# Optimization experiments

Hardware: AMD Instinct MI355X
Metric: run time of the kernel (lower is better)

## Reference

```python
import jax, jax.numpy as jnp
import numpy as np

N = 256          # number of samples (each = 3 LSTM steps)
E = 2048         # embedding dim (LSTM input size)
H = 2048         # LSTM hidden dim
CTX_VOCAB = 32
FACE_VOCAB = 1024
OUT_DIM = 2
CTX_SCALE = 1.0


def setup_inputs() -> dict:
    key = jax.random.key(0)
    ks = jax.random.split(key, 12)
    s = 0.02
    inp = {
        "ctx": jax.random.randint(ks[0], (N,), 0, CTX_VOCAB),
        "f1": jax.random.randint(ks[1], (N,), 0, FACE_VOCAB),
        "f2": jax.random.randint(ks[2], (N,), 0, FACE_VOCAB),
        "ctx_table": jax.random.normal(ks[3], (CTX_VOCAB, E), jnp.float32) * s,
        "face_table": jax.random.normal(ks[4], (FACE_VOCAB, E), jnp.float32) * s,
        "W_ih": jax.random.normal(ks[5], (4 * H, E), jnp.float32) * s,
        "W_hh": jax.random.normal(ks[6], (4 * H, H), jnp.float32) * s,
        "b_ih": jax.random.normal(ks[7], (4 * H,), jnp.float32) * s,
        "b_hh": jax.random.normal(ks[8], (4 * H,), jnp.float32) * s,
        "W_out": jax.random.normal(ks[9], (OUT_DIM, H), jnp.float32) * s,
        "b_out": jax.random.normal(ks[10], (OUT_DIM,), jnp.float32) * s,
    }
    return inp


def _lstm_scan(xs, h0, c0, W_ih, W_hh, b_ih, b_hh):
    # xs: [T, E]; single-layer LSTM, batch = 1 (vectors). PyTorch gate order i,f,g,o.
    def step(carry, x):
        h, c = carry
        gates = W_ih @ x + b_ih + W_hh @ h + b_hh  # [4H]
        i, f, g, o = jnp.split(gates, 4)
        i = jax.nn.sigmoid(i)
        f = jax.nn.sigmoid(f)
        g = jnp.tanh(g)
        o = jax.nn.sigmoid(o)
        c = f * c + i * g
        h = o * jnp.tanh(c)
        return (h, c), h

    (hF, cF), hs = jax.lax.scan(step, (h0, c0), xs)
    return hs, hF, cF  # hs: [T, H]


def reference(ctx, f1, f2, ctx_table, face_table, W_ih, W_hh, b_ih, b_hh, W_out, b_out):
    # Per-sample embeddings (batch dim of 1 in original collapses to vectors).
    ctx_e = CTX_SCALE * ctx_table[ctx]          # [N, E]
    f1_e = face_table[f1]                       # [N, E]
    f2_e = face_table[f2]                       # [N, E]
    # ctx_order == 'first': sequence per sample is [ctx, f1, f2].
    x = jnp.stack([ctx_e, f1_e, f2_e], axis=1).reshape(-1, ctx_table.shape[1])  # [3N, E]

    h0 = jnp.zeros((W_hh.shape[1],), x.dtype)
    c0 = jnp.zeros((W_hh.shape[1],), x.dtype)
    hs, hF, cF = _lstm_scan(x, h0, c0, W_ih, W_hh, b_ih, b_hh)

    # Original applies `out` to h_n after each sample (i.e., after its 3rd step).
    h_per_sample = hs[2::3]                     # [N, H]
    outputs = h_per_sample @ W_out.T + b_out    # [N, OUT_DIM]
    return outputs, hF, cF
```

## Files before the change

### kernel.cpp

```cpp
#include <hip/hip_runtime.h>
#include <hip/hip_bf16.h>
#include <stdint.h>

#define H 2048
#define FOURH 8192
#define NT 768
#define NS 256

typedef __attribute__((ext_vector_type(8))) short bf16x8;
typedef __attribute__((ext_vector_type(4))) float f32x4;
typedef __attribute__((ext_vector_type(4))) unsigned uint4v;
typedef _Float16 f16x2 __attribute__((ext_vector_type(2)));

static __device__ __forceinline__ unsigned short f2bf(float x) {
  unsigned u = __float_as_uint(x);
  return (unsigned short)((u + 0x7fffu + ((u >> 16) & 1u)) >> 16);
}
static __device__ __forceinline__ unsigned pk2(float lo, float hi) {
  return ((unsigned)f2bf(hi) << 16) | (unsigned)f2bf(lo);
}
static __device__ __forceinline__ unsigned pkf16(float lo, float hi) {
  auto h = __builtin_amdgcn_cvt_pkrtz(lo, hi);
  return __builtin_bit_cast(unsigned, h);
}
static __device__ __forceinline__ float sigm(float x) { return 1.f / (1.f + __expf(-x)); }
static __device__ __forceinline__ float tanh_fast(float x) {
  float xc = fminf(fmaxf(x, -15.f), 15.f);
  float e = __expf(2.f * xc);
  return (e - 1.f) / (e + 1.f);
}

static __device__ __forceinline__ float dot2(unsigned w, unsigned h, float acc) {
#if __has_builtin(__builtin_amdgcn_fdot2)
  return __builtin_amdgcn_fdot2(__builtin_bit_cast(f16x2, w),
                                __builtin_bit_cast(f16x2, h), acc, false);
#else
  f16x2 wv = __builtin_bit_cast(f16x2, w);
  f16x2 hv = __builtin_bit_cast(f16x2, h);
  return acc + (float)wv.x * (float)hv.x + (float)wv.y * (float)hv.y;
#endif
}

template <int PAT>
static __device__ __forceinline__ float swz(float v) {
  return __int_as_float(__builtin_amdgcn_ds_swizzle(__float_as_int(v), PAT));
}
static __device__ __forceinline__ float wave_sum(float v) {
  v += swz<0x041F>(v);
  v += swz<0x081F>(v);
  v += swz<0x101F>(v);
  v += swz<0x201F>(v);
  v += swz<0x401F>(v);
  v += __shfl_xor(v, 32, 64);
  return v;
}

__global__ void gather_x(const int* __restrict__ ctx, const int* __restrict__ f1,
                         const int* __restrict__ f2, const float* __restrict__ ctx_table,
                         const float* __restrict__ face_table, unsigned short* __restrict__ X) {
  int t = blockIdx.x;
  int s = t / 3, k = t - 3 * s;
  const float* src;
  if (k == 0)      src = ctx_table  + (size_t)ctx[s] * H;
  else if (k == 1) src = face_table + (size_t)f1[s] * H;
  else             src = face_table + (size_t)f2[s] * H;
  int c = threadIdx.x * 8;
  float4 v0 = *(const float4*)(src + c);
  float4 v1 = *(const float4*)(src + c + 4);
  uint4 o;
  o.x = pk2(v0.x, v0.y); o.y = pk2(v0.z, v0.w);
  o.z = pk2(v1.x, v1.y); o.w = pk2(v1.z, v1.w);
  *(uint4*)(X + (size_t)t * H + c) = o;
}

__launch_bounds__(256)
__global__ void gemm_p(const unsigned short* __restrict__ X, const float* __restrict__ Wih,
                       const float* __restrict__ bih, const float* __restrict__ bhh,
                       float* __restrict__ P) {
  __shared__ unsigned short Alds[128 * 32];
  __shared__ unsigned short Blds[128 * 32];
  int tid = threadIdx.x;
  int bm = (blockIdx.x >> 6) * 128;
  int bn = (blockIdx.x & 63) * 128;
  int w = tid >> 6, l = tid & 63;
  int wm = (w >> 1) * 64, wn = (w & 1) * 64;
  int sr = tid >> 1;
  int sc = (tid & 1) * 16;
  int cl = l & 15, kg = (l >> 4) * 8;

  f32x4 acc[4][4];
#pragma unroll
  for (int i = 0; i < 4; ++i)
#pragma unroll
    for (int j = 0; j < 4; ++j) acc[i][j] = (f32x4){0.f, 0.f, 0.f, 0.f};

  for (int kt = 0; kt < H; kt += 32) {
    __syncthreads();
    const unsigned short* ap = X + (size_t)(bm + sr) * H + kt + sc;
    uint4 a0 = *(const uint4*)ap;
    uint4 a1 = *(const uint4*)(ap + 8);
    const float* bp = Wih + (size_t)(bn + sr) * H + kt + sc;
    float4 f0 = *(const float4*)bp;
    float4 f1v = *(const float4*)(bp + 4);
    float4 f2v = *(const float4*)(bp + 8);
    float4 f3v = *(const float4*)(bp + 12);
    *(uint4*)(Alds + sr * 32 + sc) = a0;
    *(uint4*)(Alds + sr * 32 + sc + 8) = a1;
    uint4 b0, b1;
    b0.x = pk2(f0.x, f0.y);  b0.y = pk2(f0.z, f0.w);
    b0.z = pk2(f1v.x, f1v.y); b0.w = pk2(f1v.z, f1v.w);
    b1.x = pk2(f2v.x, f2v.y); b1.y = pk2(f2v.z, f2v.w);
    b1.z = pk2(f3v.x, f3v.y); b1.w = pk2(f3v.z, f3v.w);
    *(uint4*)(Blds + sr * 32 + sc) = b0;
    *(uint4*)(Blds + sr * 32 + sc + 8) = b1;
    __syncthreads();

    bf16x8 af[4], bb[4];
#pragma unroll
    for (int i = 0; i < 4; ++i) {
      af[i] = *(bf16x8*)(Alds + (wm + i * 16 + cl) * 32 + kg);
      bb[i] = *(bf16x8*)(Blds + (wn + i * 16 + cl) * 32 + kg);
    }
#pragma unroll
    for (int i = 0; i < 4; ++i)
#pragma unroll
      for (int j = 0; j < 4; ++j)
        acc[i][j] = __builtin_amdgcn_mfma_f32_16x16x32_bf16(af[i], bb[j], acc[i][j], 0, 0, 0);
  }

  int rg = (l >> 4) * 4;
#pragma unroll
  for (int j = 0; j < 4; ++j) {
    int n = bn + wn + j * 16 + cl;
    float bias = bih[n] + bhh[n];
#pragma unroll
    for (int i = 0; i < 4; ++i) {
      int m = bm + wm + i * 16 + rg;
#pragma unroll
      for (int r = 0; r < 4; ++r)
        P[(size_t)(m + r) * FOURH + n] = acc[i][j][r] + bias;
    }
  }
}

__launch_bounds__(256, 1)
__global__ void lstm_seq(const float* __restrict__ Whh, const float* __restrict__ P,
                         unsigned* __restrict__ hrep, float* __restrict__ hs,
                         float* __restrict__ out) {
  __shared__ float gates_lds[2][32];
  int g = blockIdx.x;
  int tid = threadIdx.x;
  int G = tid >> 6, l = tid & 63;

  unsigned wpk[8][8][2];
#pragma unroll
  for (int q = 0; q < 8; ++q) {
    const float* wrow = Whh + (size_t)(G * H + g * 8 + q) * H;
#pragma unroll
    for (int j = 0; j < 8; ++j) {
      float4 wv = *(const float4*)(wrow + j * 256 + l * 4);
      wpk[q][j][0] = pkf16(wv.x, wv.y);
      wpk[q][j][1] = pkf16(wv.z, wv.w);
    }
  }

  float c_state = 0.f;
  const unsigned* myrep = hrep + (size_t)(g & 7) * 2 * H;

  for (int t = 0; t < NT; ++t) {
    int p = t & 1;

    float p_v = 0.f;
    if (tid < 32)
      p_v = P[(size_t)t * FOURH + (size_t)(tid >> 3) * H + g * 8 + (tid & 7)];

    uint4v v0, v1, v2, v3, v4, v5, v6, v7;
    {
      const unsigned* s0 = myrep + (size_t)p * H + l * 4;
      const unsigned* s1 = s0 + 1024;
      unsigned want = ((unsigned)t & 0xffffu) << 16;
      for (;;) {
        asm volatile(
            "global_load_dwordx4 %0, %8, off sc0 sc1\n\t"
            "global_load_dwordx4 %1, %8, off offset:1024 sc0 sc1\n\t"
            "global_load_dwordx4 %2, %8, off offset:2048 sc0 sc1\n\t"
            "global_load_dwordx4 %3, %8, off offset:3072 sc0 sc1\n\t"
            "global_load_dwordx4 %4, %9, off sc0 sc1\n\t"
            "global_load_dwordx4 %5, %9, off offset:1024 sc0 sc1\n\t"
            "global_load_dwordx4 %6, %9, off offset:2048 sc0 sc1\n\t"
            "global_load_dwordx4 %7, %9, off offset:3072 sc0 sc1\n\t"
            "s_waitcnt vmcnt(0)"
            : "=&v"(v0), "=&v"(v1), "=&v"(v2), "=&v"(v3),
              "=&v"(v4), "=&v"(v5), "=&v"(v6), "=&v"(v7)
            : "v"(s0), "v"(s1)
            : "memory");
        unsigned m =
            ((v0.x ^ want) | (v0.y ^ want) | (v0.z ^ want) | (v0.w ^ want) |
             (v1.x ^ want) | (v1.y ^ want) | (v1.z ^ want) | (v1.w ^ want) |
             (v2.x ^ want) | (v2.y ^ want) | (v2.z ^ want) | (v2.w ^ want) |
             (v3.x ^ want) | (v3.y ^ want) | (v3.z ^ want) | (v3.w ^ want) |
             (v4.x ^ want) | (v4.y ^ want) | (v4.z ^ want) | (v4.w ^ want) |
             (v5.x ^ want) | (v5.y ^ want) | (v5.z ^ want) | (v5.w ^ want) |
             (v6.x ^ want) | (v6.y ^ want) | (v6.z ^ want) | (v6.w ^ want) |
             (v7.x ^ want) | (v7.y ^ want) | (v7.z ^ want) | (v7.w ^ want)) &
            0xffff0000u;
        if (m == 0) break;
        __builtin_amdgcn_s_sleep(1);
      }
    }

    float acc[8] = {0.f, 0.f, 0.f, 0.f, 0.f, 0.f, 0.f, 0.f};
#define JBLK(vj, j)                                               \
  {                                                               \
    unsigned hw0 = (vj.x & 0xffffu) | (vj.y << 16);               \
    unsigned hw1 = (vj.z & 0xffffu) | (vj.w << 16);               \
    _Pragma("unroll") for (int q = 0; q < 8; ++q) {               \
      acc[q] = dot2(wpk[q][j][0], hw0, acc[q]);                   \
      acc[q] = dot2(wpk[q][j][1], hw1, acc[q]);                   \
    }                                                             \
  }
    JBLK(v0, 0) JBLK(v1, 1) JBLK(v2, 2) JBLK(v3, 3)
    JBLK(v4, 4) JBLK(v5, 5) JBLK(v6, 6) JBLK(v7, 7)
#undef JBLK

#pragma unroll
    for (int q = 0; q < 8; ++q) acc[q] = wave_sum(acc[q]);
    if (l == 0) {
#pragma unroll
      for (int q = 0; q < 8; ++q) gates_lds[p][G * 8 + q] = acc[q];
    }
    __syncthreads();

    if (tid < 64) {
      int q = tid & 7;
      float pre_i = __shfl(p_v, q, 64);
      float pre_f = __shfl(p_v, 8 + q, 64);
      float pre_g = __shfl(p_v, 16 + q, 64);
      float pre_o = __shfl(p_v, 24 + q, 64);
      unsigned wword = 0;
      float hnew = 0.f;
      if (l < 8) {
        float iv = sigm(gates_lds[p][q]      + pre_i);
        float fv = sigm(gates_lds[p][8 + q]  + pre_f);
        float gv = tanh_fast(gates_lds[p][16 + q] + pre_g);
        float ov = sigm(gates_lds[p][24 + q] + pre_o);
        c_state = fv * c_state + iv * gv;
        hnew = ov * tanh_fast(c_state);
        wword = ((((unsigned)(t + 1)) & 0xffffu) << 16) | (pkf16(hnew, 0.f) & 0xffffu);
      }
      unsigned w0 = __shfl(wword, 0, 64), w1 = __shfl(wword, 1, 64);
      unsigned w2 = __shfl(wword, 2, 64), w3 = __shfl(wword, 3, 64);
      unsigned w4 = __shfl(wword, 4, 64), w5 = __shfl(wword, 5, 64);
      unsigned w6 = __shfl(wword, 6, 64), w7 = __shfl(wword, 7, 64);
      if (l < 8) {
        unsigned* dst = hrep + ((size_t)l * 2 + ((t + 1) & 1)) * H + g * 8;
        uint4v A, B;
        A.x = w0; A.y = w1; A.z = w2; A.w = w3;
        B.x = w4; B.y = w5; B.z = w6; B.w = w7;
        asm volatile(
            "global_store_dwordx4 %0, %2, off sc0 sc1\n\t"
            "global_store_dwordx4 %1, %3, off sc0 sc1"
            :
            : "v"(dst), "v"(dst + 4), "v"(A), "v"(B)
            : "memory");
        int m3 = t - (t / 3) * 3;
        if (m3 == 2) hs[(size_t)(t / 3) * H + g * 8 + q] = hnew;
        if (t == NT - 1) {
          out[512 + g * 8 + q] = hnew;
          out[512 + H + g * 8 + q] = c_state;
        }
      }
    }
  }
}

__global__ void out_head(const float* __restrict__ hs, const float* __restrict__ Wout,
                         const float* __restrict__ bout, float* __restrict__ out) {
  int s = blockIdx.x;
  int l = threadIdx.x;
  float a0 = 0.f, a1 = 0.f;
#pragma unroll 4
  for (int j = 0; j < 32; ++j) {
    int idx = j * 64 + l;
    float h = hs[(size_t)s * H + idx];
    a0 += h * Wout[idx];
    a1 += h * Wout[H + idx];
  }
#pragma unroll
  for (int off = 1; off < 64; off <<= 1) {
    a0 += __shfl_xor(a0, off, 64);
    a1 += __shfl_xor(a1, off, 64);
  }
  if (l == 0) {
    out[s * 2]     = a0 + bout[0];
    out[s * 2 + 1] = a1 + bout[1];
  }
}

extern "C" void kernel_launch(void* const* d_in, const int* in_sizes, int n_in,
                              void* d_out, int out_size, void* d_ws, size_t ws_size,
                              hipStream_t stream) {
  const int*   ctx        = (const int*)d_in[0];
  const int*   f1         = (const int*)d_in[1];
  const int*   f2         = (const int*)d_in[2];
  const float* ctx_table  = (const float*)d_in[3];
  const float* face_table = (const float*)d_in[4];
  const float* Wih        = (const float*)d_in[5];
  const float* Whh        = (const float*)d_in[6];
  const float* bih        = (const float*)d_in[7];
  const float* bhh        = (const float*)d_in[8];
  const float* Wout       = (const float*)d_in[9];
  const float* bout       = (const float*)d_in[10];
  float* out = (float*)d_out;

  char* ws = (char*)d_ws;
  size_t off = 0;
  unsigned short* X = (unsigned short*)(ws + off); off += (size_t)NT * H * 2;
  float* P    = (float*)(ws + off); off += (size_t)NT * FOURH * 4;
  unsigned* hrep = (unsigned*)(ws + off); off += (size_t)8 * 2 * H * 4;
  float* hs   = (float*)(ws + off); off += (size_t)NS * H * 4;

  (void)hipMemsetAsync(hrep, 0, (size_t)8 * 2 * H * 4, stream);

  gather_x<<<NT, 256, 0, stream>>>(ctx, f1, f2, ctx_table, face_table, X);
  gemm_p<<<6 * 64, 256, 0, stream>>>(X, Wih, bih, bhh, P);
  lstm_seq<<<NS, 256, 0, stream>>>(Whh, P, hrep, hs, out);
  out_head<<<NS, 64, 0, stream>>>(hs, Wout, bout, out);
}
```

Baseline: 2.194 ms.

## Give each wave all four gates for two hidden units, dropping LDS barrier

The W_hh rows held in registers are reassigned so each of the four waves owns all four gate rows for two hidden units, rather than one gate for eight units. Each wave can then apply the LSTM cell update locally with no shared-memory exchange and no __syncthreads per timestep. Each wave also writes its own two h values to the replicated hidden buffer with a dwordx2 store. The intent is to shorten the serial per-step critical path. In exchange there are four times as many small stores and flag-bearing writers per step, and c_state is now kept in wave-local lanes.

```diff
diff --git a/kernel.cpp b/kernel.cpp
--- a/kernel.cpp
+++ b/kernel.cpp
@@ -10,6 +10,7 @@
 typedef __attribute__((ext_vector_type(8))) short bf16x8;
 typedef __attribute__((ext_vector_type(4))) float f32x4;
 typedef __attribute__((ext_vector_type(4))) unsigned uint4v;
+typedef __attribute__((ext_vector_type(2))) unsigned uint2v;
 typedef _Float16 f16x2 __attribute__((ext_vector_type(2)));
 
 static __device__ __forceinline__ unsigned short f2bf(float x) {
@@ -147,7 +148,6 @@
 __global__ void lstm_seq(const float* __restrict__ Whh, const float* __restrict__ P,
                          unsigned* __restrict__ hrep, float* __restrict__ hs,
                          float* __restrict__ out) {
-  __shared__ float gates_lds[2][32];
   int g = blockIdx.x;
   int tid = threadIdx.x;
   int G = tid >> 6, l = tid & 63;
@@ -155,7 +155,7 @@
   unsigned wpk[8][8][2];
 #pragma unroll
   for (int q = 0; q < 8; ++q) {
-    const float* wrow = Whh + (size_t)(G * H + g * 8 + q) * H;
+    const float* wrow = Whh + ((size_t)(q >> 1) * H + g * 8 + 2 * G + (q & 1)) * H;
 #pragma unroll
     for (int j = 0; j < 8; ++j) {
       float4 wv = *(const float4*)(wrow + j * 256 + l * 4);
@@ -166,13 +166,14 @@
 
   float c_state = 0.f;
   const unsigned* myrep = hrep + (size_t)(g & 7) * 2 * H;
+  int row0 = g * 8 + 2 * G;
 
   for (int t = 0; t < NT; ++t) {
     int p = t & 1;
 
     float p_v = 0.f;
-    if (tid < 32)
-      p_v = P[(size_t)t * FOURH + (size_t)(tid >> 3) * H + g * 8 + (tid & 7)];
+    if (l < 8)
+      p_v = P[(size_t)t * FOURH + (size_t)(l >> 1) * H + row0 + (l & 1)];
 
     uint4v v0, v1, v2, v3, v4, v5, v6, v7;
     {
@@ -225,50 +226,42 @@
 
 #pragma unroll
     for (int q = 0; q < 8; ++q) acc[q] = wave_sum(acc[q]);
-    if (l == 0) {
-#pragma unroll
-      for (int q = 0; q < 8; ++q) gates_lds[p][G * 8 + q] = acc[q];
-    }
-    __syncthreads();
-
-    if (tid < 64) {
-      int q = tid & 7;
-      float pre_i = __shfl(p_v, q, 64);
-      float pre_f = __shfl(p_v, 8 + q, 64);
-      float pre_g = __shfl(p_v, 16 + q, 64);
-      float pre_o = __shfl(p_v, 24 + q, 64);
-      unsigned wword = 0;
-      float hnew = 0.f;
-      if (l < 8) {
-        float iv = sigm(gates_lds[p][q]      + pre_i);
-        float fv = sigm(gates_lds[p][8 + q]  + pre_f);
-        float gv = tanh_fast(gates_lds[p][16 + q] + pre_g);
-        float ov = sigm(gates_lds[p][24 + q] + pre_o);
-        c_state = fv * c_state + iv * gv;
-        hnew = ov * tanh_fast(c_state);
-        wword = ((((unsigned)(t + 1)) & 0xffffu) << 16) | (pkf16(hnew, 0.f) & 0xffffu);
-      }
-      unsigned w0 = __shfl(wword, 0, 64), w1 = __shfl(wword, 1, 64);
-      unsigned w2 = __shfl(wword, 2, 64), w3 = __shfl(wword, 3, 64);
-      unsigned w4 = __shfl(wword, 4, 64), w5 = __shfl(wword, 5, 64);
-      unsigned w6 = __shfl(wword, 6, 64), w7 = __shfl(wword, 7, 64);
-      if (l < 8) {
-        unsigned* dst = hrep + ((size_t)l * 2 + ((t + 1) & 1)) * H + g * 8;
-        uint4v A, B;
-        A.x = w0; A.y = w1; A.z = w2; A.w = w3;
-        B.x = w4; B.y = w5; B.z = w6; B.w = w7;
-        asm volatile(
-            "global_store_dwordx4 %0, %2, off sc0 sc1\n\t"
-            "global_store_dwordx4 %1, %3, off sc0 sc1"
-            :
-            : "v"(dst), "v"(dst + 4), "v"(A), "v"(B)
-            : "memory");
-        int m3 = t - (t / 3) * 3;
-        if (m3 == 2) hs[(size_t)(t / 3) * H + g * 8 + q] = hnew;
-        if (t == NT - 1) {
-          out[512 + g * 8 + q] = hnew;
-          out[512 + H + g * 8 + q] = c_state;
-        }
+
+    int r = l & 1;
+    float pi = __shfl(p_v, r, 64);
+    float pf = __shfl(p_v, 2 + r, 64);
+    float pg = __shfl(p_v, 4 + r, 64);
+    float po = __shfl(p_v, 6 + r, 64);
+    float ai = r ? acc[1] : acc[0];
+    float af = r ? acc[3] : acc[2];
+    float ag = r ? acc[5] : acc[4];
+    float ao = r ? acc[7] : acc[6];
+
+    float iv = sigm(ai + pi);
+    float fv = sigm(af + pf);
+    float gv = tanh_fast(ag + pg);
+    float ov = sigm(ao + po);
+    c_state = fv * c_state + iv * gv;
+    float hnew = ov * tanh_fast(c_state);
+    unsigned wword = ((((unsigned)(t + 1)) & 0xffffu) << 16) | (pkf16(hnew, 0.f) & 0xffffu);
+
+    unsigned u0 = __shfl(wword, 0, 64);
+    unsigned u1 = __shfl(wword, 1, 64);
+    if (l < 8) {
+      unsigned* dst = hrep + ((size_t)l * 2 + ((t + 1) & 1)) * H + row0;
+      uint2v V; V.x = u0; V.y = u1;
+      asm volatile("global_store_dwordx2 %0, %1, off sc0 sc1"
+                   :
+                   : "v"(dst), "v"(V)
+                   : "memory");
+    }
+    if (l < 2) {
+      int hidx = row0 + l;
+      int m3 = t - (t / 3) * 3;
+      if (m3 == 2) hs[(size_t)(t / 3) * H + hidx] = hnew;
+      if (t == NT - 1) {
+        out[512 + hidx] = hnew;
+        out[512 + H + hidx] = c_state;
       }
     }
   }
```

New measurement: 3.802 ms. +73.3%, slower.
